# Performance work log

Hardware: AMD Instinct MI355X
Metric: run time of the kernel (lower is better)

The kernel has to match this reference:

```python
import jax, jax.numpy as jnp
import numpy as np

INF = 100000.0
B, W, T, U, S, N = 64, 16, 64, 128, 20, 8


def setup_inputs() -> dict:
    key = jax.random.key(0)
    ks = jax.random.split(key, 9)
    xavier = (2.0 / (U + U)) ** 0.5
    return {
        "slot_utt_h": jax.random.normal(ks[0], (B, W, T, U), jnp.float32),
        "slot_candidate_c": jax.random.normal(ks[1], (S, U), jnp.float32),
        "status_candidate_c": jax.random.normal(ks[2], (N, U), jnp.float32),
        "position_encoding": jax.random.normal(ks[3], (B, W, S, U), jnp.float32),
        "q_status": jax.random.normal(ks[4], (B, W, N, U), jnp.float32),
        "mask": jnp.zeros((B, W, S * N), jnp.float32),
        "weight": jax.random.normal(ks[5], (U, U), jnp.float32) * xavier,  # bilinear co-attention weight [U,U]
        "W1": jax.random.normal(ks[6], (2 * U, U), jnp.float32) * 0.05,
        "b1": jnp.zeros((U,), jnp.float32),
        "W2": jax.random.normal(ks[7], (U, U), jnp.float32) * 0.05,
        "b2": jnp.zeros((U,), jnp.float32),
        "W3": jax.random.normal(ks[8], (U, 1), jnp.float32) * 0.05,
        "b3": jnp.zeros((1,), jnp.float32),
    }


def _zero_mask(p):
    # original: -(p == 0).float() * INF, added before softmax
    return jnp.where(p == 0.0, -INF, 0.0)


def reference(slot_utt_h, slot_candidate_c, status_candidate_c, position_encoding,
              q_status, mask, weight, W1, b1, W2, b2, W3, b3):
    # ---- attention over utterance tokens ----
    # p[b,w,s,t] = <slot_candidate_c[s], slot_utt_h[b,w,t]>
    p = jnp.einsum('su,bwtu->bwst', slot_candidate_c, slot_utt_h)
    p = jax.nn.softmax(p + _zero_mask(p), axis=-1)
    q_slot = jnp.einsum('bwst,bwtu->bwsu', p, slot_utt_h) + position_encoding  # [B,W,S,U]

    # ---- bilinear co-attention: [B,W*S,U] @ weight @ [B,U,W*N] -> [B,W,S,W,N] ----
    co = jnp.einsum('bwsu,uv,bxnv->bwsxn', q_slot, weight, q_status)
    p2 = jax.nn.softmax(co + _zero_mask(co), axis=3)  # softmax over the second window axis x

    # weighted sum of statuses over window axis x
    q_status_slot = jnp.einsum('bwsxn,bxnu->bwsnu', p2, q_status)  # [B,W,S,N,U]

    q_slot_exp = jnp.broadcast_to(q_slot[:, :, :, None, :], (B, W, S, N, U))
    features = jnp.concatenate([q_slot_exp, q_status_slot], axis=-1)  # [B,W,S,N,2U]

    # ---- MLP (dropout in eval mode = identity) ----
    h = jax.nn.relu(features @ W1 + b1)
    h = jax.nn.relu(h @ W2 + b2)
    logits = h @ W3 + b3  # [B,W,S,N,1]

    logits = logits.reshape(B, W, S * N)
    slot_pred_logits = jnp.max(logits + mask, axis=1)  # masked max-pool over window
    slot_pred_labels = (slot_pred_logits > 0.0).astype(jnp.float32)
    return (slot_pred_labels, S * N, slot_pred_logits)
```

## Files before the change

### kernel.cpp

```cpp
#include <hip/hip_runtime.h>
#include <math.h>

#define INF_ 100000.0f
constexpr int B_ = 64, W_ = 16, T_ = 64, U_ = 128, S_ = 20, N_ = 8;

typedef unsigned short ushort_t;
typedef __attribute__((ext_vector_type(8))) short bf16x8;
typedef __attribute__((ext_vector_type(4))) float floatx4;

static __device__ __forceinline__ unsigned short f2bf(float x) {
    unsigned int u = __float_as_uint(x);
    return (unsigned short)((u + 0x7fff + ((u >> 16) & 1)) >> 16);
}
static __device__ __forceinline__ float bf2f(unsigned short s) {
    return __uint_as_float(((unsigned int)s) << 16);
}

__global__ __launch_bounds__(256) void k_pre(
    const float* __restrict__ q_status, const float* __restrict__ weight,
    const float* __restrict__ W1, const float* __restrict__ W2,
    const float* __restrict__ c,
    ushort_t* __restrict__ w1topT, ushort_t* __restrict__ w2T,
    ushort_t* __restrict__ c_bf,
    ushort_t* __restrict__ Gt_bf, ushort_t* __restrict__ qs1T_bf)
{
    __shared__ __align__(16) ushort_t sw[128 * 136];
    __shared__ __align__(16) ushort_t sq[128 * 136];
    const int tid = threadIdx.x, bx = blockIdx.x;

    if (bx < 64) {
        const int b = bx;
        const float* qb = q_status + (size_t)b * 16384;
        for (int i = tid * 4; i < 16384; i += 1024) {
            int r = i >> 7, v = i & 127;
            float4 wv = *(const float4*)&weight[i];
            *(ushort4*)&sw[r * 136 + v] =
                (ushort4){f2bf(wv.x), f2bf(wv.y), f2bf(wv.z), f2bf(wv.w)};
            float4 qv = *(const float4*)&qb[i];
            *(ushort4*)&sq[r * 136 + v] =
                (ushort4){f2bf(qv.x), f2bf(qv.y), f2bf(qv.z), f2bf(qv.w)};
        }
        __syncthreads();
        const int wave = tid >> 6, lane = tid & 63, m16 = lane & 15, q = lane >> 4;
        ushort_t* Gb = Gt_bf + (size_t)b * 16384;
#pragma unroll
        for (int ci = 0; ci < 16; ++ci) {
            int tile = wave * 16 + ci;
            int mt = tile >> 3, jt = tile & 7;
            floatx4 acc = {0.f, 0.f, 0.f, 0.f};
#pragma unroll
            for (int kt = 0; kt < 4; ++kt) {
                bf16x8 a = *(const bf16x8*)&sq[(mt * 16 + m16) * 136 + kt * 32 + q * 8];
                bf16x8 w = *(const bf16x8*)&sw[(jt * 16 + m16) * 136 + kt * 32 + q * 8];
                acc = __builtin_amdgcn_mfma_f32_16x16x32_bf16(a, w, acc, 0, 0, 0);
            }
#pragma unroll
            for (int reg = 0; reg < 4; ++reg)
                Gb[(mt * 16 + q * 4 + reg) * 128 + jt * 16 + m16] = f2bf(acc[reg]);
        }
        return;
    }
    if (bx < 128) {
        const int b = bx - 64;
        const float* qb = q_status + (size_t)b * 16384;
        for (int i = tid * 4; i < 16384; i += 1024) {
            int r = i >> 7, v = i & 127;
            float4 qv = *(const float4*)&qb[i];
            *(ushort4*)&sq[r * 136 + v] =
                (ushort4){f2bf(qv.x), f2bf(qv.y), f2bf(qv.z), f2bf(qv.w)};
            int v2 = i >> 7, j = i & 127;
            float4 wv = *(const float4*)&W1[(128 + v2) * 128 + j];
            sw[(j + 0) * 136 + v2] = f2bf(wv.x);
            sw[(j + 1) * 136 + v2] = f2bf(wv.y);
            sw[(j + 2) * 136 + v2] = f2bf(wv.z);
            sw[(j + 3) * 136 + v2] = f2bf(wv.w);
        }
        __syncthreads();
        const int wave = tid >> 6, lane = tid & 63, m16 = lane & 15, q = lane >> 4;
        ushort_t* Qb = qs1T_bf + (size_t)b * 16384;
#pragma unroll
        for (int ci = 0; ci < 16; ++ci) {
            int tile = wave * 16 + ci;
            int mt = tile >> 3, jt = tile & 7;
            floatx4 acc = {0.f, 0.f, 0.f, 0.f};
#pragma unroll
            for (int kt = 0; kt < 4; ++kt) {
                bf16x8 a = *(const bf16x8*)&sq[(mt * 16 + m16) * 136 + kt * 32 + q * 8];
                bf16x8 w = *(const bf16x8*)&sw[(jt * 16 + m16) * 136 + kt * 32 + q * 8];
                acc = __builtin_amdgcn_mfma_f32_16x16x32_bf16(a, w, acc, 0, 0, 0);
            }
            ushort4 o = {f2bf(acc[0]), f2bf(acc[1]), f2bf(acc[2]), f2bf(acc[3])};
            *(ushort4*)&Qb[(jt * 16 + m16) * 128 + mt * 16 + q * 4] = o;
        }
        return;
    }
    if (bx < 144) {
        int g = (bx - 128) * 1024 + tid * 4;
        int j = g >> 7, k = g & 127;
        *(ushort4*)&w1topT[g] =
            (ushort4){f2bf(W1[k * 128 + j]), f2bf(W1[(k + 1) * 128 + j]),
                      f2bf(W1[(k + 2) * 128 + j]), f2bf(W1[(k + 3) * 128 + j])};
        return;
    }
    if (bx < 160) {
        int g = (bx - 144) * 1024 + tid * 4;
        int j = g >> 7, k = g & 127;
        *(ushort4*)&w2T[g] =
            (ushort4){f2bf(W2[k * 128 + j]), f2bf(W2[(k + 1) * 128 + j]),
                      f2bf(W2[(k + 2) * 128 + j]), f2bf(W2[(k + 3) * 128 + j])};
        return;
    }
    for (int i = tid * 4; i < 4096; i += 1024) {
        int s = i >> 7;
        ushort4 o = {0, 0, 0, 0};
        if (s < 20) {
            float4 v = *(const float4*)&c[i];
            o = (ushort4){f2bf(v.x), f2bf(v.y), f2bf(v.z), f2bf(v.w)};
        }
        *(ushort4*)&c_bf[i] = o;
    }
}

__global__ __launch_bounds__(640, 5) void k_main(
    const float* __restrict__ h,
    const ushort_t* __restrict__ c_bf,
    const float* __restrict__ pos,
    const ushort_t* __restrict__ Gt_bf,
    const ushort_t* __restrict__ qs1T_bf,
    const ushort_t* __restrict__ w1topT,
    const float* __restrict__ b1,
    const ushort_t* __restrict__ w2T,
    const float* __restrict__ b2,
    const float* __restrict__ W3,
    const float* __restrict__ b3,
    float* __restrict__ lg)
{
    __shared__ __align__(16) ushort_t sh[39168];

    const int bw = blockIdx.x, b = bw >> 4, tid = threadIdx.x;
    const int wave = tid >> 6, lane = tid & 63, m16 = lane & 15, q = lane >> 4;

    const float* hb = h + (size_t)bw * 8192;
    for (int i = tid * 4; i < 8192; i += 2560) {
        int t = i >> 7, u = i & 127;
        float4 v = *(const float4*)&hb[i];
        ushort4 o = {f2bf(v.x), f2bf(v.y), f2bf(v.z), f2bf(v.w)};
        *(ushort4*)&sh[t * 136 + u] = o;
        sh[8704 + (u + 0) * 72 + t] = o.x;
        sh[8704 + (u + 1) * 72 + t] = o.y;
        sh[8704 + (u + 2) * 72 + t] = o.z;
        sh[8704 + (u + 3) * 72 + t] = o.w;
    }
    for (int i = tid; i < 2304; i += 640) sh[22272 + i] = 0;
    __syncthreads();

    {
        float* sc = (float*)sh + 8960;
        if (wave < 8) {
            int mt = wave >> 2, jt = wave & 3;
            floatx4 acc = {0.f, 0.f, 0.f, 0.f};
#pragma unroll
            for (int kt = 0; kt < 4; ++kt) {
                bf16x8 a = *(const bf16x8*)&c_bf[(mt * 16 + m16) * 128 + kt * 32 + q * 8];
                bf16x8 bb = *(const bf16x8*)&sh[(jt * 16 + m16) * 136 + kt * 32 + q * 8];
                acc = __builtin_amdgcn_mfma_f32_16x16x32_bf16(a, bb, acc, 0, 0, 0);
            }
#pragma unroll
            for (int reg = 0; reg < 4; ++reg)
                sc[(mt * 16 + q * 4 + reg) * 68 + jt * 16 + m16] = acc[reg];
        }
    }
    __syncthreads();

    {
        const float* sc = (const float*)sh + 8960;
        for (int s = wave; s < 20; s += 10) {
            float v = sc[s * 68 + lane];
            if (v == 0.0f) v = -INF_;
            float m = v;
            for (int d = 32; d; d >>= 1) m = fmaxf(m, __shfl_xor(m, d));
            float e = expf(v - m);
            float sum = e;
            for (int d = 32; d; d >>= 1) sum += __shfl_xor(sum, d);
            sh[22272 + s * 72 + lane] = f2bf(e / sum);
        }
    }
    __syncthreads();

    if (wave < 8) {
        const size_t obase = (size_t)bw * 2560;
#pragma unroll
        for (int ci = 0; ci < 2; ++ci) {
            int cmb = wave * 2 + ci;
            int mt = cmb >> 3, jt = cmb & 7;
            floatx4 acc = {0.f, 0.f, 0.f, 0.f};
#pragma unroll
            for (int kt = 0; kt < 2; ++kt) {
                bf16x8 a = *(const bf16x8*)&sh[22272 + (mt * 16 + m16) * 72 + kt * 32 + q * 8];
                bf16x8 bb = *(const bf16x8*)&sh[8704 + (jt * 16 + m16) * 72 + kt * 32 + q * 8];
                acc = __builtin_amdgcn_mfma_f32_16x16x32_bf16(a, bb, acc, 0, 0, 0);
            }
            int u = jt * 16 + m16;
#pragma unroll
            for (int reg = 0; reg < 4; ++reg) {
                int row = mt * 16 + q * 4 + reg;
                if (row < 20)
                    sh[17920 + row * 136 + u] =
                        f2bf(acc[reg] + pos[obase + row * 128 + u]);
            }
        }
    }
    __syncthreads();

    for (int i = tid * 4; i < 16384; i += 2560) {
        int r = i >> 7, k2 = i & 127;
        *(ushort4*)&sh[r * 136 + k2] = *(const ushort4*)&qs1T_bf[(size_t)b * 16384 + i];
    }
    {
        const bf16x8 zz = {0, 0, 0, 0, 0, 0, 0, 0};
        float* Af = (float*)sh + 13776;
        const ushort_t* Gb = Gt_bf + (size_t)b * 16384;
        for (int t = wave; t < 32; t += 10) {
            int isA = t >> 4, tt = t & 15;
            int mt = tt >> 3, jt = tt & 7;
            int arow = mt * 16 + m16;
            const ushort_t* Bsrc = isA ? w1topT : Gb;
            floatx4 acc = {0.f, 0.f, 0.f, 0.f};
#pragma unroll
            for (int kt = 0; kt < 4; ++kt) {
                bf16x8 a = (arow < 20)
                    ? *(const bf16x8*)&sh[17920 + arow * 136 + kt * 32 + q * 8] : zz;
                bf16x8 g = *(const bf16x8*)&Bsrc[(jt * 16 + m16) * 128 + kt * 32 + q * 8];
                acc = __builtin_amdgcn_mfma_f32_16x16x32_bf16(a, g, acc, 0, 0, 0);
            }
            int col = jt * 16 + m16;
            if (isA) {
                float bv = b1[col];
#pragma unroll
                for (int reg = 0; reg < 4; ++reg) {
                    int row = mt * 16 + q * 4 + reg;
                    if (row < 20) Af[row * 132 + col] = acc[reg] + bv;
                }
            } else {
#pragma unroll
                for (int reg = 0; reg < 4; ++reg) {
                    int row = mt * 16 + q * 4 + reg;
                    if (row < 20) sh[22272 + row * 132 + col] = f2bf(acc[reg]);
                }
            }
        }
    }
    __syncthreads();

    {
        int sn = tid >> 2, xi = tid & 3;
        int s = sn >> 3, n = sn & 7;
        const ushort_t* crow = &sh[22272 + s * 132];
        float v[4];
        float m = -INFINITY;
#pragma unroll
        for (int j = 0; j < 4; ++j) {
            float t = bf2f(crow[(xi + 4 * j) * 8 + n]);
            if (t == 0.0f) t = -INF_;
            v[j] = t;
            m = fmaxf(m, t);
        }
        m = fmaxf(m, __shfl_xor(m, 1));
        m = fmaxf(m, __shfl_xor(m, 2));
        float sum = 0.f;
#pragma unroll
        for (int j = 0; j < 4; ++j) { v[j] = expf(v[j] - m); sum += v[j]; }
        sum += __shfl_xor(sum, 1);
        sum += __shfl_xor(sum, 2);
        float r = 1.0f / sum;
#pragma unroll
        for (int j = 0; j < 4; ++j)
            sh[24912 + s * 132 + (xi + 4 * j) * 8 + n] = f2bf(v[j] * r);
    }
    __syncthreads();

    const int n = m16 & 7;
    const int sIdx = wave * 2 + (m16 >> 3);
    const int rowS = wave * 16 + m16;

    floatx4 gacc[8];
#pragma unroll
    for (int mt = 0; mt < 8; ++mt) gacc[mt] = (floatx4){0.f, 0.f, 0.f, 0.f};
#pragma unroll
    for (int kt = 0; kt < 4; ++kt) {
        short pv = (short)sh[24912 + sIdx * 132 + kt * 32 + q * 8 + n];
        bf16x8 pf = {0, 0, 0, 0, 0, 0, 0, 0};
        pf[0] = (n == 0) ? pv : (short)0;
        pf[1] = (n == 1) ? pv : (short)0;
        pf[2] = (n == 2) ? pv : (short)0;
        pf[3] = (n == 3) ? pv : (short)0;
        pf[4] = (n == 4) ? pv : (short)0;
        pf[5] = (n == 5) ? pv : (short)0;
        pf[6] = (n == 6) ? pv : (short)0;
        pf[7] = (n == 7) ? pv : (short)0;
#pragma unroll
        for (int mt = 0; mt < 8; ++mt) {
            bf16x8 af = *(const bf16x8*)&sh[(mt * 16 + m16) * 136 + kt * 32 + q * 8];
            gacc[mt] = __builtin_amdgcn_mfma_f32_16x16x32_bf16(af, pf, gacc[mt], 0, 0, 0);
        }
    }
    __syncthreads();

    {
        const float* Af = (const float*)sh + 13776 + sIdx * 132;
#pragma unroll
        for (int mt = 0; mt < 8; ++mt) {
            int u0 = mt * 16 + q * 4;
            float4 av = *(const float4*)&Af[u0];
            ushort4 o;
            o.x = f2bf(fmaxf(gacc[mt][0] + av.x, 0.f));
            o.y = f2bf(fmaxf(gacc[mt][1] + av.y, 0.f));
            o.z = f2bf(fmaxf(gacc[mt][2] + av.z, 0.f));
            o.w = f2bf(fmaxf(gacc[mt][3] + av.w, 0.f));
            *(ushort4*)&sh[rowS * 136 + u0] = o;
        }
    }
    __syncthreads();

    for (int i = tid * 4; i < 16384; i += 2560) {
        int r = i >> 7, k2 = i & 127;
        *(ushort4*)&sh[21760 + r * 136 + k2] = *(const ushort4*)&w2T[i];
    }
    __syncthreads();

    floatx4 acc[8];
#pragma unroll
    for (int jt = 0; jt < 8; ++jt) acc[jt] = (floatx4){0.f, 0.f, 0.f, 0.f};
#pragma unroll
    for (int kt = 0; kt < 4; ++kt) {
        const int k0 = kt * 32 + q * 8;
        bf16x8 af = *(const bf16x8*)&sh[rowS * 136 + k0];
#pragma unroll
        for (int jt = 0; jt < 8; ++jt) {
            bf16x8 bfr = *(const bf16x8*)&sh[21760 + (jt * 16 + m16) * 136 + k0];
            acc[jt] = __builtin_amdgcn_mfma_f32_16x16x32_bf16(af, bfr, acc[jt], 0, 0, 0);
        }
    }

    float b2v[8], w3v[8];
#pragma unroll
    for (int jt = 0; jt < 8; ++jt) {
        b2v[jt] = b2[jt * 16 + m16];
        w3v[jt] = W3[jt * 16 + m16];
    }
    const float b3v = b3[0];

#pragma unroll
    for (int reg = 0; reg < 4; ++reg) {
        float p = 0.f;
#pragma unroll
        for (int jt = 0; jt < 8; ++jt)
            p += fmaxf(acc[jt][reg] + b2v[jt], 0.f) * w3v[jt];
        p += __shfl_xor(p, 1);
        p += __shfl_xor(p, 2);
        p += __shfl_xor(p, 4);
        p += __shfl_xor(p, 8);
        if (m16 == 0)
            lg[(size_t)bw * 160 + wave * 16 + q * 4 + reg] = p + b3v;
    }
}

__global__ __launch_bounds__(256) void k5_final(
    const float* __restrict__ lg,
    const float* __restrict__ mask,
    float* __restrict__ out)
{
    int idx = blockIdx.x * 256 + threadIdx.x;
    const int SN = S_ * N_;
    if (idx < B_ * SN) {
        int b = idx / SN, sn = idx % SN;
        float m = -INFINITY;
        for (int w = 0; w < W_; ++w) {
            float v = lg[((size_t)b * W_ + w) * SN + sn] + mask[((size_t)b * W_ + w) * SN + sn];
            m = fmaxf(m, v);
        }
        out[idx] = (m > 0.f) ? 1.f : 0.f;
        out[B_ * SN + 1 + idx] = m;
    }
    if (idx == 0) out[B_ * SN] = (float)SN;
}

extern "C" void kernel_launch(void* const* d_in, const int* in_sizes, int n_in,
                              void* d_out, int out_size, void* d_ws, size_t ws_size,
                              hipStream_t stream) {
    const float* slot_utt_h = (const float*)d_in[0];
    const float* slot_candidate_c = (const float*)d_in[1];
    const float* position_encoding = (const float*)d_in[3];
    const float* q_status = (const float*)d_in[4];
    const float* mask = (const float*)d_in[5];
    const float* weight = (const float*)d_in[6];
    const float* W1 = (const float*)d_in[7];
    const float* b1 = (const float*)d_in[8];
    const float* W2 = (const float*)d_in[9];
    const float* b2 = (const float*)d_in[10];
    const float* W3 = (const float*)d_in[11];
    const float* b3 = (const float*)d_in[12];
    float* out = (float*)d_out;

    float* f = (float*)d_ws;
    float*    lg       = f + 0;
    ushort_t* Gt_bf    = (ushort_t*)(f + 163840);
    ushort_t* qs1T_bf  = (ushort_t*)(f + 688128);
    ushort_t* w1topT   = (ushort_t*)(f + 1212416);
    ushort_t* w2T      = (ushort_t*)(f + 1220608);
    ushort_t* c_bf     = (ushort_t*)(f + 1228800);

    k_pre<<<161, 256, 0, stream>>>(q_status, weight, W1, W2,
                                   slot_candidate_c,
                                   w1topT, w2T, c_bf, Gt_bf, qs1T_bf);
    k_main<<<1024, 640, 0, stream>>>(slot_utt_h, c_bf, position_encoding,
                                     Gt_bf, qs1T_bf, w1topT, b1, w2T,
                                     b2, W3, b3, lg);
    k5_final<<<(B_ * S_ * N_ + 255) / 256, 256, 0, stream>>>(lg, mask, out);
}
```

Before: 187.8 us.

## Split fused main kernel into attention, projection and MLP kernels

The single large k_main is split into three kernels. kA computes token attention and q_slot, kB runs the co-attention and W1-top projections as dense 64-row tiles that share a cached B matrix per batch, and kC does the status softmax and MLP. kC passes the first MLP layer's activations to the second GEMM through lane shuffles instead of shared memory, which drops some barriers. The aim is to stop wasting MFMA work on padded 20-row tiles and to reduce per-block shared memory and idle waves. In exchange it adds intermediate global round-trips for q_slot, co and A, plus extra kernel launches.

Result: faster. 178.9 us (-4.8%).

```diff
diff --git a/kernel.cpp b/kernel.cpp
--- a/kernel.cpp
+++ b/kernel.cpp
@@ -121,146 +121,189 @@
     }
 }
 
-__global__ __launch_bounds__(640, 5) void k_main(
+__global__ __launch_bounds__(256) void kA(
     const float* __restrict__ h,
     const ushort_t* __restrict__ c_bf,
     const float* __restrict__ pos,
+    ushort_t* __restrict__ q_slot_bf)
+{
+    __shared__ __align__(16) ushort_t sh_hT[128 * 72];
+    __shared__ __align__(16) float    sh_sc[32 * 68];
+    __shared__ __align__(16) ushort_t sh_P[32 * 72];
+
+    const int bw = blockIdx.x, tid = threadIdx.x;
+    const int wave = tid >> 6, lane = tid & 63, m16 = lane & 15, q = lane >> 4;
+    const float* hb = h + (size_t)bw * 8192;
+
+    for (int i = tid * 4; i < 8192; i += 1024) {
+        int t = i >> 7, u = i & 127;
+        float4 v = *(const float4*)&hb[i];
+        sh_hT[(u + 0) * 72 + t] = f2bf(v.x);
+        sh_hT[(u + 1) * 72 + t] = f2bf(v.y);
+        sh_hT[(u + 2) * 72 + t] = f2bf(v.z);
+        sh_hT[(u + 3) * 72 + t] = f2bf(v.w);
+    }
+    for (int i = tid; i < 2304; i += 256) sh_P[i] = 0;
+
+#pragma unroll
+    for (int ci = 0; ci < 2; ++ci) {
+        int cmb = wave * 2 + ci;
+        int mt = cmb >> 2, jt = cmb & 3;
+        floatx4 acc = {0.f, 0.f, 0.f, 0.f};
+#pragma unroll
+        for (int kt = 0; kt < 4; ++kt) {
+            bf16x8 a = *(const bf16x8*)&c_bf[(mt * 16 + m16) * 128 + kt * 32 + q * 8];
+            const float* hp = &hb[(jt * 16 + m16) * 128 + kt * 32 + q * 8];
+            float4 b0 = *(const float4*)&hp[0];
+            float4 b1v = *(const float4*)&hp[4];
+            bf16x8 bb;
+            bb[0] = (short)f2bf(b0.x); bb[1] = (short)f2bf(b0.y);
+            bb[2] = (short)f2bf(b0.z); bb[3] = (short)f2bf(b0.w);
+            bb[4] = (short)f2bf(b1v.x); bb[5] = (short)f2bf(b1v.y);
+            bb[6] = (short)f2bf(b1v.z); bb[7] = (short)f2bf(b1v.w);
+            acc = __builtin_amdgcn_mfma_f32_16x16x32_bf16(a, bb, acc, 0, 0, 0);
+        }
+#pragma unroll
+        for (int reg = 0; reg < 4; ++reg)
+            sh_sc[(mt * 16 + q * 4 + reg) * 68 + jt * 16 + m16] = acc[reg];
+    }
+    __syncthreads();
+
+    for (int s = wave; s < 20; s += 4) {
+        float v = sh_sc[s * 68 + lane];
+        if (v == 0.0f) v = -INF_;
+        float m = v;
+        for (int d = 32; d; d >>= 1) m = fmaxf(m, __shfl_xor(m, d));
+        float e = expf(v - m);
+        float sum = e;
+        for (int d = 32; d; d >>= 1) sum += __shfl_xor(sum, d);
+        sh_P[s * 72 + lane] = f2bf(e / sum);
+    }
+    __syncthreads();
+
+    const size_t obase = (size_t)bw * 2560;
+#pragma unroll
+    for (int ci = 0; ci < 4; ++ci) {
+        int cmb = wave * 4 + ci;
+        int mt = cmb >> 3, jt = cmb & 7;
+        floatx4 acc = {0.f, 0.f, 0.f, 0.f};
+#pragma unroll
+        for (int kt = 0; kt < 2; ++kt) {
+            bf16x8 a = *(const bf16x8*)&sh_P[(mt * 16 + m16) * 72 + kt * 32 + q * 8];
+            bf16x8 b = *(const bf16x8*)&sh_hT[(jt * 16 + m16) * 72 + kt * 32 + q * 8];
+            acc = __builtin_amdgcn_mfma_f32_16x16x32_bf16(a, b, acc, 0, 0, 0);
+        }
+        int u = jt * 16 + m16;
+#pragma unroll
+        for (int reg = 0; reg < 4; ++reg) {
+            int row = mt * 16 + q * 4 + reg;
+            if (row < 20)
+                q_slot_bf[obase + row * 128 + u] =
+                    f2bf(acc[reg] + pos[obase + row * 128 + u]);
+        }
+    }
+}
+
+__global__ __launch_bounds__(256) void kB(
+    const ushort_t* __restrict__ q_slot_bf,
     const ushort_t* __restrict__ Gt_bf,
-    const ushort_t* __restrict__ qs1T_bf,
     const ushort_t* __restrict__ w1topT,
     const float* __restrict__ b1,
+    ushort_t* __restrict__ co_bf,
+    float* __restrict__ A)
+{
+    __shared__ __align__(16) ushort_t shB[128 * 136];
+    const int tid = threadIdx.x, bx = blockIdx.x;
+    const int wave = tid >> 6, lane = tid & 63, m16 = lane & 15, q = lane >> 4;
+
+    if (bx < 320) {
+        const int b = bx / 5, rt = bx - b * 5;
+        for (int i = tid * 4; i < 16384; i += 1024)
+            *(ushort4*)&shB[(i >> 7) * 136 + (i & 127)] =
+                *(const ushort4*)&Gt_bf[(size_t)b * 16384 + i];
+        __syncthreads();
+
+        const size_t rbase = (size_t)b * 320 + rt * 64 + wave * 16;
+        floatx4 acc[8];
+#pragma unroll
+        for (int jt = 0; jt < 8; ++jt) acc[jt] = (floatx4){0.f, 0.f, 0.f, 0.f};
+#pragma unroll
+        for (int kt = 0; kt < 4; ++kt) {
+            bf16x8 a = *(const bf16x8*)&q_slot_bf[(rbase + m16) * 128 + kt * 32 + q * 8];
+#pragma unroll
+            for (int jt = 0; jt < 8; ++jt) {
+                bf16x8 g = *(const bf16x8*)&shB[(jt * 16 + m16) * 136 + kt * 32 + q * 8];
+                acc[jt] = __builtin_amdgcn_mfma_f32_16x16x32_bf16(a, g, acc[jt], 0, 0, 0);
+            }
+        }
+#pragma unroll
+        for (int jt = 0; jt < 8; ++jt)
+#pragma unroll
+            for (int reg = 0; reg < 4; ++reg)
+                co_bf[(rbase + q * 4 + reg) * 128 + jt * 16 + m16] = f2bf(acc[jt][reg]);
+    } else {
+        const int blk = bx - 320;
+        for (int i = tid * 4; i < 16384; i += 1024)
+            *(ushort4*)&shB[(i >> 7) * 136 + (i & 127)] =
+                *(const ushort4*)&w1topT[i];
+        __syncthreads();
+
+        const size_t rbase = (size_t)blk * 64 + wave * 16;
+        floatx4 acc[8];
+#pragma unroll
+        for (int jt = 0; jt < 8; ++jt) acc[jt] = (floatx4){0.f, 0.f, 0.f, 0.f};
+#pragma unroll
+        for (int kt = 0; kt < 4; ++kt) {
+            bf16x8 a = *(const bf16x8*)&q_slot_bf[(rbase + m16) * 128 + kt * 32 + q * 8];
+#pragma unroll
+            for (int jt = 0; jt < 8; ++jt) {
+                bf16x8 g = *(const bf16x8*)&shB[(jt * 16 + m16) * 136 + kt * 32 + q * 8];
+                acc[jt] = __builtin_amdgcn_mfma_f32_16x16x32_bf16(a, g, acc[jt], 0, 0, 0);
+            }
+        }
+#pragma unroll
+        for (int jt = 0; jt < 8; ++jt) {
+            int col = jt * 16 + m16;
+            float bv = b1[col];
+#pragma unroll
+            for (int reg = 0; reg < 4; ++reg)
+                A[(rbase + q * 4 + reg) * 128 + col] = acc[jt][reg] + bv;
+        }
+    }
+}
+
+__global__ __launch_bounds__(640, 5) void kC(
+    const ushort_t* __restrict__ co_bf,
+    const ushort_t* __restrict__ qs1T_bf,
+    const float* __restrict__ A,
     const ushort_t* __restrict__ w2T,
     const float* __restrict__ b2,
     const float* __restrict__ W3,
     const float* __restrict__ b3,
     float* __restrict__ lg)
 {
-    __shared__ __align__(16) ushort_t sh[39168];
+    __shared__ __align__(16) ushort_t shQ[128 * 136];
+    __shared__ __align__(16) ushort_t shW[128 * 136];
+    __shared__ __align__(16) ushort_t shP[20 * 132];
 
     const int bw = blockIdx.x, b = bw >> 4, tid = threadIdx.x;
     const int wave = tid >> 6, lane = tid & 63, m16 = lane & 15, q = lane >> 4;
 
-    const float* hb = h + (size_t)bw * 8192;
-    for (int i = tid * 4; i < 8192; i += 2560) {
-        int t = i >> 7, u = i & 127;
-        float4 v = *(const float4*)&hb[i];
-        ushort4 o = {f2bf(v.x), f2bf(v.y), f2bf(v.z), f2bf(v.w)};
-        *(ushort4*)&sh[t * 136 + u] = o;
-        sh[8704 + (u + 0) * 72 + t] = o.x;
-        sh[8704 + (u + 1) * 72 + t] = o.y;
-        sh[8704 + (u + 2) * 72 + t] = o.z;
-        sh[8704 + (u + 3) * 72 + t] = o.w;
-    }
-    for (int i = tid; i < 2304; i += 640) sh[22272 + i] = 0;
-    __syncthreads();
-
-    {
-        float* sc = (float*)sh + 8960;
-        if (wave < 8) {
-            int mt = wave >> 2, jt = wave & 3;
-            floatx4 acc = {0.f, 0.f, 0.f, 0.f};
-#pragma unroll
-            for (int kt = 0; kt < 4; ++kt) {
-                bf16x8 a = *(const bf16x8*)&c_bf[(mt * 16 + m16) * 128 + kt * 32 + q * 8];
-                bf16x8 bb = *(const bf16x8*)&sh[(jt * 16 + m16) * 136 + kt * 32 + q * 8];
-                acc = __builtin_amdgcn_mfma_f32_16x16x32_bf16(a, bb, acc, 0, 0, 0);
-            }
-#pragma unroll
-            for (int reg = 0; reg < 4; ++reg)
-                sc[(mt * 16 + q * 4 + reg) * 68 + jt * 16 + m16] = acc[reg];
-        }
-    }
-    __syncthreads();
-
-    {
-        const float* sc = (const float*)sh + 8960;
-        for (int s = wave; s < 20; s += 10) {
-            float v = sc[s * 68 + lane];
-            if (v == 0.0f) v = -INF_;
-            float m = v;
-            for (int d = 32; d; d >>= 1) m = fmaxf(m, __shfl_xor(m, d));
-            float e = expf(v - m);
-            float sum = e;
-            for (int d = 32; d; d >>= 1) sum += __shfl_xor(sum, d);
-            sh[22272 + s * 72 + lane] = f2bf(e / sum);
-        }
-    }
-    __syncthreads();
-
-    if (wave < 8) {
-        const size_t obase = (size_t)bw * 2560;
-#pragma unroll
-        for (int ci = 0; ci < 2; ++ci) {
-            int cmb = wave * 2 + ci;
-            int mt = cmb >> 3, jt = cmb & 7;
-            floatx4 acc = {0.f, 0.f, 0.f, 0.f};
-#pragma unroll
-            for (int kt = 0; kt < 2; ++kt) {
-                bf16x8 a = *(const bf16x8*)&sh[22272 + (mt * 16 + m16) * 72 + kt * 32 + q * 8];
-                bf16x8 bb = *(const bf16x8*)&sh[8704 + (jt * 16 + m16) * 72 + kt * 32 + q * 8];
-                acc = __builtin_amdgcn_mfma_f32_16x16x32_bf16(a, bb, acc, 0, 0, 0);
-            }
-            int u = jt * 16 + m16;
-#pragma unroll
-            for (int reg = 0; reg < 4; ++reg) {
-                int row = mt * 16 + q * 4 + reg;
-                if (row < 20)
-                    sh[17920 + row * 136 + u] =
-                        f2bf(acc[reg] + pos[obase + row * 128 + u]);
-            }
-        }
-    }
-    __syncthreads();
-
     for (int i = tid * 4; i < 16384; i += 2560) {
-        int r = i >> 7, k2 = i & 127;
-        *(ushort4*)&sh[r * 136 + k2] = *(const ushort4*)&qs1T_bf[(size_t)b * 16384 + i];
-    }
-    {
-        const bf16x8 zz = {0, 0, 0, 0, 0, 0, 0, 0};
-        float* Af = (float*)sh + 13776;
-        const ushort_t* Gb = Gt_bf + (size_t)b * 16384;
-        for (int t = wave; t < 32; t += 10) {
-            int isA = t >> 4, tt = t & 15;
-            int mt = tt >> 3, jt = tt & 7;
-            int arow = mt * 16 + m16;
-            const ushort_t* Bsrc = isA ? w1topT : Gb;
-            floatx4 acc = {0.f, 0.f, 0.f, 0.f};
-#pragma unroll
-            for (int kt = 0; kt < 4; ++kt) {
-                bf16x8 a = (arow < 20)
-                    ? *(const bf16x8*)&sh[17920 + arow * 136 + kt * 32 + q * 8] : zz;
-                bf16x8 g = *(const bf16x8*)&Bsrc[(jt * 16 + m16) * 128 + kt * 32 + q * 8];
-                acc = __builtin_amdgcn_mfma_f32_16x16x32_bf16(a, g, acc, 0, 0, 0);
-            }
-            int col = jt * 16 + m16;
-            if (isA) {
-                float bv = b1[col];
-#pragma unroll
-                for (int reg = 0; reg < 4; ++reg) {
-                    int row = mt * 16 + q * 4 + reg;
-                    if (row < 20) Af[row * 132 + col] = acc[reg] + bv;
-                }
-            } else {
-#pragma unroll
-                for (int reg = 0; reg < 4; ++reg) {
-                    int row = mt * 16 + q * 4 + reg;
-                    if (row < 20) sh[22272 + row * 132 + col] = f2bf(acc[reg]);
-                }
-            }
-        }
-    }
-    __syncthreads();
+        int r = i >> 7, k = i & 127;
+        *(ushort4*)&shQ[r * 136 + k] = *(const ushort4*)&qs1T_bf[(size_t)b * 16384 + i];
+        *(ushort4*)&shW[r * 136 + k] = *(const ushort4*)&w2T[i];
+    }
 
     {
         int sn = tid >> 2, xi = tid & 3;
-        int s = sn >> 3, n = sn & 7;
-        const ushort_t* crow = &sh[22272 + s * 132];
+        int s = sn >> 3, n2 = sn & 7;
+        const ushort_t* crow = co_bf + ((size_t)bw * 20 + s) * 128;
         float v[4];
         float m = -INFINITY;
 #pragma unroll
         for (int j = 0; j < 4; ++j) {
-            float t = bf2f(crow[(xi + 4 * j) * 8 + n]);
+            float t = bf2f(crow[(xi + 4 * j) * 8 + n2]);
             if (t == 0.0f) t = -INF_;
             v[j] = t;
             m = fmaxf(m, t);
@@ -275,20 +318,19 @@
         float r = 1.0f / sum;
 #pragma unroll
         for (int j = 0; j < 4; ++j)
-            sh[24912 + s * 132 + (xi + 4 * j) * 8 + n] = f2bf(v[j] * r);
+            shP[s * 132 + (xi + 4 * j) * 8 + n2] = f2bf(v[j] * r);
     }
     __syncthreads();
 
     const int n = m16 & 7;
     const int sIdx = wave * 2 + (m16 >> 3);
-    const int rowS = wave * 16 + m16;
 
     floatx4 gacc[8];
 #pragma unroll
     for (int mt = 0; mt < 8; ++mt) gacc[mt] = (floatx4){0.f, 0.f, 0.f, 0.f};
 #pragma unroll
     for (int kt = 0; kt < 4; ++kt) {
-        short pv = (short)sh[24912 + sIdx * 132 + kt * 32 + q * 8 + n];
+        short pv = (short)shP[sIdx * 132 + kt * 32 + q * 8 + n];
         bf16x8 pf = {0, 0, 0, 0, 0, 0, 0, 0};
         pf[0] = (n == 0) ? pv : (short)0;
         pf[1] = (n == 1) ? pv : (short)0;
@@ -300,45 +342,55 @@
         pf[7] = (n == 7) ? pv : (short)0;
 #pragma unroll
         for (int mt = 0; mt < 8; ++mt) {
-            bf16x8 af = *(const bf16x8*)&sh[(mt * 16 + m16) * 136 + kt * 32 + q * 8];
+            bf16x8 af = *(const bf16x8*)&shQ[(mt * 16 + m16) * 136 + kt * 32 + q * 8];
             gacc[mt] = __builtin_amdgcn_mfma_f32_16x16x32_bf16(af, pf, gacc[mt], 0, 0, 0);
         }
     }
-    __syncthreads();
-
+
+    unsigned int h1u[8][2];
     {
-        const float* Af = (const float*)sh + 13776 + sIdx * 132;
+        const float* Ab = A + ((size_t)bw * 20 + sIdx) * 128;
 #pragma unroll
         for (int mt = 0; mt < 8; ++mt) {
             int u0 = mt * 16 + q * 4;
-            float4 av = *(const float4*)&Af[u0];
-            ushort4 o;
-            o.x = f2bf(fmaxf(gacc[mt][0] + av.x, 0.f));
-            o.y = f2bf(fmaxf(gacc[mt][1] + av.y, 0.f));
-            o.z = f2bf(fmaxf(gacc[mt][2] + av.z, 0.f));
-            o.w = f2bf(fmaxf(gacc[mt][3] + av.w, 0.f));
-            *(ushort4*)&sh[rowS * 136 + u0] = o;
-        }
-    }
-    __syncthreads();
-
-    for (int i = tid * 4; i < 16384; i += 2560) {
-        int r = i >> 7, k2 = i & 127;
-        *(ushort4*)&sh[21760 + r * 136 + k2] = *(const ushort4*)&w2T[i];
-    }
-    __syncthreads();
+            float4 av = *(const float4*)&Ab[u0];
+            unsigned int x0 = f2bf(fmaxf(gacc[mt][0] + av.x, 0.f));
+            unsigned int x1 = f2bf(fmaxf(gacc[mt][1] + av.y, 0.f));
+            unsigned int x2 = f2bf(fmaxf(gacc[mt][2] + av.z, 0.f));
+            unsigned int x3 = f2bf(fmaxf(gacc[mt][3] + av.w, 0.f));
+            h1u[mt][0] = x0 | (x1 << 16);
+            h1u[mt][1] = x2 | (x3 << 16);
+        }
+    }
 
     floatx4 acc[8];
 #pragma unroll
     for (int jt = 0; jt < 8; ++jt) acc[jt] = (floatx4){0.f, 0.f, 0.f, 0.f};
+
+    const int sl0 = m16 + 16 * ((2 * q) & 3);
+    const int sl1 = m16 + 16 * ((2 * q + 1) & 3);
+    const bool hi = (q & 2);
 #pragma unroll
     for (int kt = 0; kt < 4; ++kt) {
+        int wa0 = __shfl((int)h1u[kt * 2 + 0][0], sl0);
+        int wb0 = __shfl((int)h1u[kt * 2 + 1][0], sl0);
+        int wa1 = __shfl((int)h1u[kt * 2 + 0][1], sl0);
+        int wb1 = __shfl((int)h1u[kt * 2 + 1][1], sl0);
+        int wa2 = __shfl((int)h1u[kt * 2 + 0][0], sl1);
+        int wb2 = __shfl((int)h1u[kt * 2 + 1][0], sl1);
+        int wa3 = __shfl((int)h1u[kt * 2 + 0][1], sl1);
+        int wb3 = __shfl((int)h1u[kt * 2 + 1][1], sl1);
+        int4 fr;
+        fr.x = hi ? wb0 : wa0;
+        fr.y = hi ? wb1 : wa1;
+        fr.z = hi ? wb2 : wa2;
+        fr.w = hi ? wb3 : wa3;
+        bf16x8 af2 = *(bf16x8*)&fr;
         const int k0 = kt * 32 + q * 8;
-        bf16x8 af = *(const bf16x8*)&sh[rowS * 136 + k0];
 #pragma unroll
         for (int jt = 0; jt < 8; ++jt) {
-            bf16x8 bfr = *(const bf16x8*)&sh[21760 + (jt * 16 + m16) * 136 + k0];
-            acc[jt] = __builtin_amdgcn_mfma_f32_16x16x32_bf16(af, bfr, acc[jt], 0, 0, 0);
+            bf16x8 bfr = *(const bf16x8*)&shW[(jt * 16 + m16) * 136 + k0];
+            acc[jt] = __builtin_amdgcn_mfma_f32_16x16x32_bf16(af2, bfr, acc[jt], 0, 0, 0);
         }
     }
 
@@ -349,7 +401,6 @@
         w3v[jt] = W3[jt * 16 + m16];
     }
     const float b3v = b3[0];
-
 #pragma unroll
     for (int reg = 0; reg < 4; ++reg) {
         float p = 0.f;
@@ -403,18 +454,21 @@
     float* out = (float*)d_out;
 
     float* f = (float*)d_ws;
-    float*    lg       = f + 0;
-    ushort_t* Gt_bf    = (ushort_t*)(f + 163840);
-    ushort_t* qs1T_bf  = (ushort_t*)(f + 688128);
-    ushort_t* w1topT   = (ushort_t*)(f + 1212416);
-    ushort_t* w2T      = (ushort_t*)(f + 1220608);
-    ushort_t* c_bf     = (ushort_t*)(f + 1228800);
+    float*    lg        = f + 0;
+    float*    A         = f + 163840;
+    ushort_t* q_slot_bf = (ushort_t*)(f + 2785280);
+    ushort_t* co_bf     = (ushort_t*)(f + 4096000);
+    ushort_t* Gt_bf     = (ushort_t*)(f + 5406720);
+    ushort_t* qs1T_bf   = (ushort_t*)(f + 5931008);
+    ushort_t* w1topT    = (ushort_t*)(f + 6455296);
+    ushort_t* w2T       = (ushort_t*)(f + 6463488);
+    ushort_t* c_bf      = (ushort_t*)(f + 6471680);
 
     k_pre<<<161, 256, 0, stream>>>(q_status, weight, W1, W2,
                                    slot_candidate_c,
                                    w1topT, w2T, c_bf, Gt_bf, qs1T_bf);
-    k_main<<<1024, 640, 0, stream>>>(slot_utt_h, c_bf, position_encoding,
-                                     Gt_bf, qs1T_bf, w1topT, b1, w2T,
-                                     b2, W3, b3, lg);
+    kA<<<1024, 256, 0, stream>>>(slot_utt_h, c_bf, position_encoding, q_slot_bf);
+    kB<<<640, 256, 0, stream>>>(q_slot_bf, Gt_bf, w1topT, b1, co_bf, A);
+    kC<<<1024, 640, 0, stream>>>(co_bf, qs1T_bf, A, w2T, b2, W3, b3, lg);
     k5_final<<<(B_ * S_ * N_ + 255) / 256, 256, 0, stream>>>(lg, mask, out);
 }
```
